# Optimization experiments

Hardware: AMD Instinct MI355X
Metric: run time of the kernel (lower is better)

Reference implementation:

```python
import jax, jax.numpy as jnp
import numpy as np

N, E, IN, HID, OUT, H, NCLS = 20000, 320000, 128, 32, 8, 8, 10

def _ln(x, g, b, eps=1e-5):
    mu = x.mean(-1, keepdims=True)
    var = ((x - mu) ** 2).mean(-1, keepdims=True)
    return g * (x - mu) / jnp.sqrt(var + eps) + b

def _gelu(x):
    return jax.nn.gelu(x, approximate=False)

def _tconv(x, src, dst, Wq, bq, Wk, bk, Wv, bv, Ws, bs, heads):
    # PyG TransformerConv, concat=True, root_weight=True, lin_beta is None
    n = x.shape[0]
    C = Wq.shape[1] // heads
    q = (x @ Wq + bq).reshape(n, heads, C)
    k = (x @ Wk + bk).reshape(n, heads, C)
    v = (x @ Wv + bv).reshape(n, heads, C)
    logits = (q[dst] * k[src]).sum(-1) / jnp.sqrt(jnp.asarray(C, x.dtype))  # [E,H]
    m = jax.lax.stop_gradient(jax.ops.segment_max(logits, dst, num_segments=n))
    e = jnp.exp(logits - m[dst])
    denom = jax.ops.segment_sum(e, dst, num_segments=n)
    alpha = e / (denom[dst] + 1e-16)  # per-target-node edge softmax
    agg = jax.ops.segment_sum(alpha[:, :, None] * v[src], dst, num_segments=n)
    out = agg.reshape(n, heads * C) + x @ Ws + bs
    return out, alpha

def _forward(src, dst, x,
             c1_Wq, c1_bq, c1_Wk, c1_bk, c1_Wv, c1_bv, c1_Ws, c1_bs,
             c2_Wq, c2_bq, c2_Wk, c2_bk, c2_Wv, c2_bv, c2_Ws, c2_bs,
             c3_Wq, c3_bq, c3_Wk, c3_bk, c3_Wv, c3_bv, c3_Ws, c3_bs,
             c4_Wq, c4_bq, c4_Wk, c4_bk, c4_Wv, c4_bv, c4_Ws, c4_bs,
             n1_g, n1_b, n2_g, n2_b, n3_g, n3_b, n4_g, n4_b,
             fc_W, fc_b):
    h1 = _ln(_gelu(_tconv(x, src, dst, c1_Wq, c1_bq, c1_Wk, c1_bk, c1_Wv, c1_bv, c1_Ws, c1_bs, H)[0]), n1_g, n1_b)
    h2_raw, attn = _tconv(h1, src, dst, c2_Wq, c2_bq, c2_Wk, c2_bk, c2_Wv, c2_bv, c2_Ws, c2_bs, H)
    h2 = _ln(_gelu(h2_raw), n2_g, n2_b)
    h3 = _ln(_gelu(_tconv(h2, src, dst, c3_Wq, c3_bq, c3_Wk, c3_bk, c3_Wv, c3_bv, c3_Ws, c3_bs, H)[0]), n3_g, n3_b)
    h4 = _ln(_gelu(_tconv(h3, src, dst, c4_Wq, c4_bq, c4_Wk, c4_bk, c4_Wv, c4_bv, c4_Ws, c4_bs, 1)[0]), n4_g, n4_b)
    x_out = h2 @ fc_W + fc_b
    return x_out, h4, attn

def setup_inputs() -> dict:
    key = jax.random.key(0)
    ks = iter(jax.random.split(key, 64))
    def p(shape, s=0.05):
        return jax.random.normal(next(ks), shape, dtype=jnp.float32) * s
    inp = {}
    inp['x'] = jax.random.normal(next(ks), (N, IN), dtype=jnp.float32)
    inp['edge_index'] = jax.random.randint(next(ks), (2, E), 0, N, dtype=jnp.int32)
    dims = [('c1', IN, H * HID), ('c2', H * HID, H * OUT), ('c3', H * OUT, H * HID), ('c4', H * HID, IN)]
    for name, di, do in dims:
        for w in ['Wq', 'Wk', 'Wv', 'Ws']:
            inp[name + '_' + w] = p((di, do))
        for bnm in ['bq', 'bk', 'bv', 'bs']:
            inp[name + '_' + bnm] = jnp.zeros((do,), jnp.float32)
    for nm, d in [('n1', H * HID), ('n2', H * OUT), ('n3', H * HID), ('n4', IN)]:
        inp[nm + '_g'] = jnp.ones((d,), jnp.float32)
        inp[nm + '_b'] = jnp.zeros((d,), jnp.float32)
    inp['fc_W'] = p((H * OUT, NCLS))
    inp['fc_b'] = jnp.zeros((NCLS,), jnp.float32)
    return inp

def reference(x, edge_index,
              c1_Wq, c1_bq, c1_Wk, c1_bk, c1_Wv, c1_bv, c1_Ws, c1_bs,
              c2_Wq, c2_bq, c2_Wk, c2_bk, c2_Wv, c2_bv, c2_Ws, c2_bs,
              c3_Wq, c3_bq, c3_Wk, c3_bk, c3_Wv, c3_bv, c3_Ws, c3_bs,
              c4_Wq, c4_bq, c4_Wk, c4_bk, c4_Wv, c4_bv, c4_Ws, c4_bs,
              n1_g, n1_b, n2_g, n2_b, n3_g, n3_b, n4_g, n4_b,
              fc_W, fc_b):
    src, dst = edge_index[0], edge_index[1]
    return _forward(src, dst, x,
                    c1_Wq, c1_bq, c1_Wk, c1_bk, c1_Wv, c1_bv, c1_Ws, c1_bs,
                    c2_Wq, c2_bq, c2_Wk, c2_bk, c2_Wv, c2_bv, c2_Ws, c2_bs,
                    c3_Wq, c3_bq, c3_Wk, c3_bk, c3_Wv, c3_bv, c3_Ws, c3_bs,
                    c4_Wq, c4_bq, c4_Wk, c4_bk, c4_Wv, c4_bv, c4_Ws, c4_bs,
                    n1_g, n1_b, n2_g, n2_b, n3_g, n3_b, n4_g, n4_b,
                    fc_W, fc_b)
```

## Files before the change

### kernel.cpp

```cpp
#include <hip/hip_runtime.h>
#include <hip/hip_bf16.h>
#include <math.h>

#define NN 20000
#define MP 20032
#define NE 320000

typedef __hip_bfloat16 bf16;
typedef __attribute__((ext_vector_type(8))) short short8v;
typedef __attribute__((ext_vector_type(4))) short short4v;
typedef __attribute__((ext_vector_type(4))) float f32x4;

__device__ __forceinline__ float b2f(bf16 v){ return __bfloat162float(v); }
__device__ __forceinline__ bf16 f2b(float v){ return __float2bfloat16(v); }
__device__ __forceinline__ float bfbits(short s){
  return __uint_as_float(((unsigned)(unsigned short)s) << 16);
}
__device__ __forceinline__ int clampi(int v, int lo, int hi){ return v < lo ? lo : (v > hi ? hi : v); }
__device__ __forceinline__ void stv(bf16* p, float v){ *p = f2b(v); }
__device__ __forceinline__ void stv(float* p, float v){ *p = v; }
__device__ __forceinline__ float ldv(const bf16* p){ return b2f(*p); }
__device__ __forceinline__ float ldv(const float* p){ return *p; }

template<int CPL>
__device__ __forceinline__ void ldrow(const bf16* p, float* o){
  if constexpr (CPL == 8){
    short8v v = *reinterpret_cast<const short8v*>(p);
#pragma unroll
    for (int j = 0; j < 8; j++) o[j] = bfbits(v[j]);
  } else {
    short4v v = *reinterpret_cast<const short4v*>(p);
#pragma unroll
    for (int j = 0; j < 4; j++) o[j] = bfbits(v[j]);
  }
}

__device__ __forceinline__ short8v ldA8(const bf16* p){
  return *reinterpret_cast<const short8v*>(p);
}
__device__ __forceinline__ short8v ldA8(const float* p){
  float4 a0 = *reinterpret_cast<const float4*>(p);
  float4 a1 = *reinterpret_cast<const float4*>(p + 4);
  short8v r;
  bf16 b;
  b = f2b(a0.x); r[0] = *(const short*)&b;
  b = f2b(a0.y); r[1] = *(const short*)&b;
  b = f2b(a0.z); r[2] = *(const short*)&b;
  b = f2b(a0.w); r[3] = *(const short*)&b;
  b = f2b(a1.x); r[4] = *(const short*)&b;
  b = f2b(a1.y); r[5] = *(const short*)&b;
  b = f2b(a1.z); r[6] = *(const short*)&b;
  b = f2b(a1.w); r[7] = *(const short*)&b;
  return r;
}

__global__ void fill_k(float* __restrict__ out, int n, float val){
  int i = blockIdx.x*blockDim.x + threadIdx.x;
  if (i < n) out[i] = val;
}

__global__ void pack_w(const float* __restrict__ W, bf16* __restrict__ Wp, int K, int D){
  int i = blockIdx.x*256 + threadIdx.x;
  if (i >= K*D) return;
  int j = i & 7, l = (i >> 3) & 63;
  int TG = D >> 4;
  int tg = (i >> 9) % TG, s = (i >> 9) / TG;
  int k = s*32 + (l >> 4)*8 + j, n = tg*16 + (l & 15);
  Wp[i] = f2b(W[(size_t)k*D + n]);
}

template<typename AT, typename TS>
__global__ void gemm_qkvs(const AT* __restrict__ X,
    const short8v* __restrict__ WQ, const short8v* __restrict__ WK,
    const short8v* __restrict__ WV, const short8v* __restrict__ WS,
    const float* __restrict__ bQ, const float* __restrict__ bK,
    const float* __restrict__ bV, const float* __restrict__ bS,
    bf16* __restrict__ Qo, bf16* __restrict__ Ko, bf16* __restrict__ Vo,
    TS* __restrict__ So,
    int K, int TG, int tg0, int ldQKV, int ldS, int ocolS, int MstoreS){
  int w = threadIdx.x >> 6, lane = threadIdx.x & 63;
  int n0 = blockIdx.x*64;
  size_t m0 = (size_t)blockIdx.y*64 + w*16;
  int lr = lane & 15, lk = lane >> 4;
  int ar = clampi((int)(m0 + lr), 0, NN-1);
  const AT* xp = X + (size_t)ar*K + lk*8;
  size_t wo = ((size_t)(tg0 + (n0 >> 4)))*64 + lane;
  f32x4 acc[4][4];
#pragma unroll
  for (int j = 0; j < 4; j++)
#pragma unroll
    for (int t = 0; t < 4; t++) acc[j][t] = f32x4{0,0,0,0};
  int steps = K >> 5;
  for (int s = 0; s < steps; s++){
    short8v a = ldA8(xp + s*32);
    size_t ro = wo + (size_t)s*TG*64;
#pragma unroll
    for (int t = 0; t < 4; t++){
      size_t idx = ro + t*64;
      acc[0][t] = __builtin_amdgcn_mfma_f32_16x16x32_bf16(a, WQ[idx], acc[0][t], 0, 0, 0);
      acc[1][t] = __builtin_amdgcn_mfma_f32_16x16x32_bf16(a, WK[idx], acc[1][t], 0, 0, 0);
      acc[2][t] = __builtin_amdgcn_mfma_f32_16x16x32_bf16(a, WV[idx], acc[2][t], 0, 0, 0);
      acc[3][t] = __builtin_amdgcn_mfma_f32_16x16x32_bf16(a, WS[idx], acc[3][t], 0, 0, 0);
    }
  }
#pragma unroll
  for (int t = 0; t < 4; t++){
    int col = n0 + t*16 + lr;
    float b0 = bQ[col], b1 = bK[col], b2 = bV[col], b3 = bS[col];
#pragma unroll
    for (int r = 0; r < 4; r++){
      size_t row = m0 + lk*4 + r;
      Qo[row*ldQKV + col] = f2b(acc[0][t][r] + b0);
      Ko[row*ldQKV + col] = f2b(acc[1][t][r] + b1);
      Vo[row*ldQKV + col] = f2b(acc[2][t][r] + b2);
      if ((int)row < MstoreS) stv(&So[row*(size_t)ldS + ocolS + col], acc[3][t][r] + b3);
    }
  }
}

__global__ void count_k(const int* __restrict__ ei, int* __restrict__ cnt, int E){
  int e = blockIdx.x*blockDim.x + threadIdx.x;
  if (e < E){
    int d = clampi(ei[E + e], 0, NN-1);
    atomicAdd(&cnt[d], 1);
  }
}

__global__ void exscan_k(const int* __restrict__ cnt, int* __restrict__ off, int n){
  __shared__ int wtot[16];
  __shared__ int carrysh;
  int tid = threadIdx.x, lane = tid & 63, w = tid >> 6;
  if (tid == 0) carrysh = 0;
  __syncthreads();
  for (int base = 0; base < n; base += 1024){
    int i = base + tid;
    int v = (i < n) ? cnt[i] : 0;
    int s = v;
#pragma unroll
    for (int d = 1; d < 64; d <<= 1){
      int t = __shfl_up(s, d);
      if (lane >= d) s += t;
    }
    if (lane == 63) wtot[w] = s;
    __syncthreads();
    int woff = 0;
    for (int j = 0; j < w; j++) woff += wtot[j];
    int c = carrysh;
    if (i < n) off[i] = c + woff + s - v;
    __syncthreads();
    if (tid == 1023) carrysh = c + woff + s;
    __syncthreads();
  }
  if (threadIdx.x == 0) off[n] = carrysh;
}

__global__ void scatter_k(const int* __restrict__ ei, int* __restrict__ cur,
                          int* __restrict__ perm, int* __restrict__ srcs, int E){
  int e = blockIdx.x*blockDim.x + threadIdx.x;
  if (e >= E) return;
  int s = clampi(ei[e], 0, NN-1);
  int d = clampi(ei[E + e], 0, NN-1);
  int p = atomicAdd(&cur[d], 1);
  if (p >= 0 && p < E){ perm[p] = e; srcs[p] = s; }
}

template<int D, int H, typename TO>
__global__ void fused_attn(const bf16* __restrict__ Q, const bf16* __restrict__ Kf,
                           const bf16* __restrict__ V, const int* __restrict__ srcs,
                           const int* __restrict__ offs,
                           TO* __restrict__ Xout, int ldO, int col0,
                           bf16* __restrict__ LOG, float* __restrict__ MxO,
                           float* __restrict__ DnO, float scale){
  constexpr int CPL = D/16;
  constexpr int LPH = 16/H;
  int node = blockIdx.x*4 + (threadIdx.x >> 6);
  if (node >= NN) return;
  int lane = threadIdx.x & 63;
  int hl = lane & 15;
  int slot = lane >> 4;
  float q[CPL];
  {
    float tmp[CPL];
    ldrow<CPL>(Q + (size_t)node*D + hl*CPL, tmp);
#pragma unroll
    for (int j = 0; j < CPL; j++) q[j] = tmp[j] * scale;
  }
  float m = -INFINITY, den = 0.f;
  float acc[CPL];
#pragma unroll
  for (int j = 0; j < CPL; j++) acc[j] = 0.f;
  int s0 = offs[node], e0 = offs[node+1];
  int i = s0 + slot;
  bool vcur = i < e0;
  int sc = vcur ? srcs[i] : 0;
  float kc[CPL], vc[CPL];
  ldrow<CPL>(Kf + (size_t)sc*D + hl*CPL, kc);
  ldrow<CPL>(V  + (size_t)sc*D + hl*CPL, vc);
  int iters = (e0 - s0 + 3) >> 2;
  for (int it = 0; it < iters; ++it){
    int inext = i + 4;
    bool vnxt = inext < e0;
    int sn = vnxt ? srcs[inext] : 0;
    float kn[CPL], vn[CPL];
    ldrow<CPL>(Kf + (size_t)sn*D + hl*CPL, kn);
    ldrow<CPL>(V  + (size_t)sn*D + hl*CPL, vn);
    float t = 0.f;
#pragma unroll
    for (int j = 0; j < CPL; j++) t += q[j]*kc[j];
#pragma unroll
    for (int o = 1; o < LPH; o <<= 1) t += __shfl_xor(t, o);
    if (!vcur) t = -INFINITY;
    if (LOG && vcur && ((hl & (LPH-1)) == 0)) LOG[(size_t)i*H + hl/LPH] = f2b(t);
    float tm = fmaxf(t, __shfl_xor(t, 16));
    tm = fmaxf(tm, __shfl_xor(tm, 32));
    float nm = fmaxf(m, tm);
    float fe = __expf(m - nm);
    float pe = __expf(t - nm);
    den = den*fe + pe;
#pragma unroll
    for (int j = 0; j < CPL; j++) acc[j] = acc[j]*fe + pe*vc[j];
    m = nm;
    vcur = vnxt; i = inext;
#pragma unroll
    for (int j = 0; j < CPL; j++){ kc[j] = kn[j]; vc[j] = vn[j]; }
  }
  den += __shfl_xor(den, 16);
  den += __shfl_xor(den, 32);
#pragma unroll
  for (int j = 0; j < CPL; j++){
    acc[j] += __shfl_xor(acc[j], 16);
    acc[j] += __shfl_xor(acc[j], 32);
  }
  float inv = 1.f/(den + 1e-16f);
  if (slot == 0){
    TO* o = Xout + (size_t)node*ldO + col0 + hl*CPL;
#pragma unroll
    for (int j = 0; j < CPL; j++) stv(&o[j], ldv(&o[j]) + acc[j]*inv);
    if (MxO && ((hl & (LPH-1)) == 0)){
      MxO[node*H + hl/LPH] = m;
      DnO[node*H + hl/LPH] = den;
    }
  }
}

__global__ void alpha8_k(const bf16* __restrict__ LOG, const float* __restrict__ Mx,
                         const float* __restrict__ Dn, const int* __restrict__ ei,
                         const int* __restrict__ perm, float* __restrict__ attn){
  size_t t = (size_t)blockIdx.x*blockDim.x + threadIdx.x;
  if (t >= (size_t)NE*8) return;
  int pos = (int)(t >> 3), h = (int)(t & 7);
  int e = perm[pos];
  int node = ei[NE + e];
  float a = __expf(b2f(LOG[t]) - Mx[node*8 + h]) / (Dn[node*8 + h] + 1e-16f);
  attn[(size_t)e*8 + h] = a;
}

template<int CPL, typename T>
__global__ void gelu_ln(T* __restrict__ X, const float* __restrict__ G,
                        const float* __restrict__ Bt){
  int node = blockIdx.x*4 + (threadIdx.x >> 6);
  if (node >= NN) return;
  constexpr int D = CPL*64;
  int lane = threadIdx.x & 63;
  T* xr = X + (size_t)node*D + lane*CPL;
  float v[CPL]; float s = 0.f;
#pragma unroll
  for (int j = 0; j < CPL; j++){
    float t = ldv(&xr[j]);
    float ge = 0.5f*t*(1.f + erff(t*0.70710678118654752f));
    v[j] = ge; s += ge;
  }
#pragma unroll
  for (int off = 1; off < 64; off <<= 1) s += __shfl_xor(s, off);
  float mu = s * (1.f/D);
  float q = 0.f;
#pragma unroll
  for (int j = 0; j < CPL; j++){ float d = v[j]-mu; q += d*d; }
#pragma unroll
  for (int off = 1; off < 64; off <<= 1) q += __shfl_xor(q, off);
  float inv = 1.f / sqrtf(q*(1.f/D) + 1e-5f);
#pragma unroll
  for (int j = 0; j < CPL; j++){
    int c = lane*CPL + j;
    stv(&xr[j], G[c]*(v[j]-mu)*inv + Bt[c]);
  }
}

__global__ void fc_k(const bf16* __restrict__ X, const float* __restrict__ W,
                     const float* __restrict__ B, float* __restrict__ Out,
                     int K, int D){
  int m = blockIdx.x*4 + (threadIdx.x >> 6);
  int lane = threadIdx.x & 63;
  if (m >= NN || lane >= D) return;
  float acc = B[lane];
  for (int k = 0; k < K; k++) acc += b2f(X[(size_t)m*K + k]) * W[(size_t)k*D + lane];
  Out[(size_t)m*D + lane] = acc;
}

extern "C" void kernel_launch(void* const* d_in, const int* in_sizes, int n_in,
                              void* d_out, int out_size, void* d_ws, size_t ws_size,
                              hipStream_t stream){
  int code = 0;
  if (n_in != 44) code = 100;
  else {
    const int wsz[4] = {32768,16384,16384,32768};
    const int bsz[4] = {256,64,256,128};
    bool ok = in_sizes[0] == NN*128 && in_sizes[1] == 2*NE
           && in_sizes[42] == 640 && in_sizes[43] == 10;
    for (int l = 0; l < 4 && ok; l++){
      for (int j = 0; j < 4; j++)
        ok = ok && in_sizes[2+l*8+j] == wsz[l] && in_sizes[2+l*8+4+j] == bsz[l];
      ok = ok && in_sizes[34+2*l] == bsz[l] && in_sizes[35+2*l] == bsz[l];
    }
    if (!ok) code = 140;
  }
  if (code){
    fill_k<<<((size_t)out_size+255)/256, 256, 0, stream>>>((float*)d_out, out_size, (float)code);
    return;
  }

  const float* x = (const float*)d_in[0];
  const int*   ei = (const int*)d_in[1];
  const float *W[4][4], *Bw[4][4], *lng[4], *lnb[4];
  for (int l = 0; l < 4; l++){
    for (int j = 0; j < 4; j++){
      W[l][j]  = (const float*)d_in[2 + l*8 + j];
      Bw[l][j] = (const float*)d_in[2 + l*8 + 4 + j];
    }
    lng[l] = (const float*)d_in[34 + 2*l];
    lnb[l] = (const float*)d_in[35 + 2*l];
  }
  const float* fcW = (const float*)d_in[42];
  const float* fcB = (const float*)d_in[43];

  char* ws = (char*)d_ws;
  size_t o = 0;
  auto alloc = [&](size_t bytes)->void*{ void* p = ws + o; o += (bytes + 255)/256*256; return p; };
  bf16* Hb   = (bf16*)alloc((size_t)MP*256*2);
  bf16* H2b  = (bf16*)alloc((size_t)MP*64*2);
  int* OFFS  = (int*)alloc((size_t)(NN+1)*4);
  int* PERM  = (int*)alloc((size_t)NE*4);
  int* SRCS  = (int*)alloc((size_t)NE*4);
  char* AR   = (char*)alloc((size_t)3*MP*128*2);
  bf16* WPK  = (bf16*)alloc((size_t)393216*2);
  size_t need = o;
  bf16* Qc = (bf16*)AR;
  bf16* Kc = (bf16*)(AR + (size_t)MP*128*2);
  bf16* Vc = (bf16*)(AR + (size_t)2*MP*128*2);
  int*  CURS = (int*)AR;
  bf16* q2  = (bf16*)AR;
  bf16* k2  = (bf16*)(AR + (size_t)MP*64*2);
  bf16* v2  = (bf16*)(AR + (size_t)2*MP*64*2);
  bf16* LOG = (bf16*)(AR + (size_t)3*MP*64*2);
  float* Mx = (float*)(AR + (size_t)3*MP*64*2 + (size_t)NE*8*2);
  float* Dn = (float*)((char*)Mx + (size_t)NN*8*4);

  float* out_x  = (float*)d_out;
  float* out_h4 = out_x + (size_t)NN*10;
  float* out_at = out_h4 + (size_t)NN*128;

  if (ws_size < need){
    fill_k<<<((size_t)out_size+255)/256, 256, 0, stream>>>((float*)d_out, out_size, 160.0f);
    return;
  }

  const int KD[4] = {128,256,64,256};
  const int DD[4] = {256,64,256,128};
  bf16* Wp[4][4];
  {
    size_t off = 0;
    for (int l = 0; l < 4; l++)
      for (int j = 0; j < 4; j++){
        Wp[l][j] = WPK + off;
        int kd = KD[l]*DD[l];
        pack_w<<<(kd+255)/256, 256, 0, stream>>>(W[l][j], Wp[l][j], KD[l], DD[l]);
        off += kd;
      }
  }

  hipMemsetAsync(CURS, 0, (size_t)NN*4, stream);
  count_k<<<NE/256, 256, 0, stream>>>(ei, CURS, NE);
  exscan_k<<<1, 1024, 0, stream>>>(CURS, OFFS, NN);
  hipMemcpyAsync(CURS, OFFS, (size_t)NN*4, hipMemcpyDeviceToDevice, stream);
  scatter_k<<<NE/256, 256, 0, stream>>>(ei, CURS, PERM, SRCS, NE);

  const float s32  = 0.1767766952966369f;
  const float s8   = 0.3535533905932738f;
  const float s128 = 0.0883883476483184f;
  const dim3 gm64(1, MP/64), gm128(2, MP/64);

  for (int col = 0; col <= 128; col += 128){
    int tg0 = col >> 4;
    gemm_qkvs<float,bf16><<<gm128,256,0,stream>>>(x,
        (const short8v*)Wp[0][0], (const short8v*)Wp[0][1],
        (const short8v*)Wp[0][2], (const short8v*)Wp[0][3],
        Bw[0][0]+col, Bw[0][1]+col, Bw[0][2]+col, Bw[0][3]+col,
        Qc, Kc, Vc, Hb, 128, 16, tg0, 128, 256, col, MP);
    fused_attn<128,4,bf16><<<NN/4,256,0,stream>>>(Qc,Kc,Vc, SRCS,OFFS, Hb,256,col,
                                                  nullptr,nullptr,nullptr, s32);
  }
  gelu_ln<4><<<NN/4,256,0,stream>>>(Hb, lng[0], lnb[0]);

  gemm_qkvs<bf16,bf16><<<gm64,256,0,stream>>>(Hb,
      (const short8v*)Wp[1][0], (const short8v*)Wp[1][1],
      (const short8v*)Wp[1][2], (const short8v*)Wp[1][3],
      Bw[1][0], Bw[1][1], Bw[1][2], Bw[1][3],
      q2, k2, v2, H2b, 256, 4, 0, 64, 64, 0, MP);
  fused_attn<64,8,bf16><<<NN/4,256,0,stream>>>(q2,k2,v2, SRCS,OFFS, H2b,64,0,
                                               LOG,Mx,Dn, s8);
  alpha8_k<<<NE*8/256,256,0,stream>>>(LOG, Mx, Dn, ei, PERM, out_at);
  gelu_ln<1><<<NN/4,256,0,stream>>>(H2b, lng[1], lnb[1]);

  fc_k<<<NN/4,256,0,stream>>>(H2b, fcW, fcB, out_x, 64, 10);

  for (int col = 0; col <= 128; col += 128){
    int tg0 = col >> 4;
    gemm_qkvs<bf16,bf16><<<gm128,256,0,stream>>>(H2b,
        (const short8v*)Wp[2][0], (const short8v*)Wp[2][1],
        (const short8v*)Wp[2][2], (const short8v*)Wp[2][3],
        Bw[2][0]+col, Bw[2][1]+col, Bw[2][2]+col, Bw[2][3]+col,
        Qc, Kc, Vc, Hb, 64, 16, tg0, 128, 256, col, MP);
    fused_attn<128,4,bf16><<<NN/4,256,0,stream>>>(Qc,Kc,Vc, SRCS,OFFS, Hb,256,col,
                                                  nullptr,nullptr,nullptr, s32);
  }
  gelu_ln<4><<<NN/4,256,0,stream>>>(Hb, lng[2], lnb[2]);

  gemm_qkvs<bf16,float><<<gm128,256,0,stream>>>(Hb,
      (const short8v*)Wp[3][0], (const short8v*)Wp[3][1],
      (const short8v*)Wp[3][2], (const short8v*)Wp[3][3],
      Bw[3][0], Bw[3][1], Bw[3][2], Bw[3][3],
      Qc, Kc, Vc, out_h4, 256, 8, 0, 128, 128, 0, NN);
  fused_attn<128,1,float><<<NN/4,256,0,stream>>>(Qc,Kc,Vc, SRCS,OFFS, out_h4,128,0,
                                                 nullptr,nullptr,nullptr, s128);
  gelu_ln<2><<<NN/4,256,0,stream>>>(out_h4, lng[3], lnb[3]);
}
```

Measured before the change: 398.2 us.

## Process full 256-wide layers in single passes and batch weight packing

Layers 1 and 3 previously ran as two 128-column halves, each with its own GEMM and attention pass. They now use one GEMM over all 256 columns and one fused attention with D=256 and CPL=16, so each edge's source indices, offsets and loop overhead are traversed once instead of twice. The 16 per-weight pack launches become a single pack_all launch, and the exscan writes the cursor array directly, which drops a device copy. Dedicated Q/K/V buffers replace the aliased scratch area, at the cost of more workspace and a higher register load per lane in attention.

New measurement: 364.4 us. -8.5%, faster.

```diff
diff --git a/kernel.cpp b/kernel.cpp
--- a/kernel.cpp
+++ b/kernel.cpp
@@ -24,7 +24,12 @@
 
 template<int CPL>
 __device__ __forceinline__ void ldrow(const bf16* p, float* o){
-  if constexpr (CPL == 8){
+  if constexpr (CPL == 16){
+    short8v v0 = *reinterpret_cast<const short8v*>(p);
+    short8v v1 = *reinterpret_cast<const short8v*>(p + 8);
+#pragma unroll
+    for (int j = 0; j < 8; j++){ o[j] = bfbits(v0[j]); o[8+j] = bfbits(v1[j]); }
+  } else if constexpr (CPL == 8){
     short8v v = *reinterpret_cast<const short8v*>(p);
 #pragma unroll
     for (int j = 0; j < 8; j++) o[j] = bfbits(v[j]);
@@ -59,14 +64,22 @@
   if (i < n) out[i] = val;
 }
 
-__global__ void pack_w(const float* __restrict__ W, bf16* __restrict__ Wp, int K, int D){
+struct PackArgs {
+  const float* w[16];
+  unsigned long long off[16];
+  int K[16];
+  int D[16];
+};
+__global__ void pack_all(PackArgs pa, bf16* __restrict__ out){
+  int wi = blockIdx.y;
+  int K = pa.K[wi], D = pa.D[wi];
   int i = blockIdx.x*256 + threadIdx.x;
   if (i >= K*D) return;
   int j = i & 7, l = (i >> 3) & 63;
   int TG = D >> 4;
   int tg = (i >> 9) % TG, s = (i >> 9) / TG;
   int k = s*32 + (l >> 4)*8 + j, n = tg*16 + (l & 15);
-  Wp[i] = f2b(W[(size_t)k*D + n]);
+  out[pa.off[wi] + i] = f2b(pa.w[wi][(size_t)k*D + n]);
 }
 
 template<typename AT, typename TS>
@@ -77,14 +90,14 @@
     const float* __restrict__ bV, const float* __restrict__ bS,
     bf16* __restrict__ Qo, bf16* __restrict__ Ko, bf16* __restrict__ Vo,
     TS* __restrict__ So,
-    int K, int TG, int tg0, int ldQKV, int ldS, int ocolS, int MstoreS){
+    int K, int TG, int ldQKV, int ldS, int MstoreS){
   int w = threadIdx.x >> 6, lane = threadIdx.x & 63;
   int n0 = blockIdx.x*64;
   size_t m0 = (size_t)blockIdx.y*64 + w*16;
   int lr = lane & 15, lk = lane >> 4;
   int ar = clampi((int)(m0 + lr), 0, NN-1);
   const AT* xp = X + (size_t)ar*K + lk*8;
-  size_t wo = ((size_t)(tg0 + (n0 >> 4)))*64 + lane;
+  size_t wo = ((size_t)(n0 >> 4))*64 + lane;
   f32x4 acc[4][4];
 #pragma unroll
   for (int j = 0; j < 4; j++)
@@ -113,7 +126,7 @@
       Qo[row*ldQKV + col] = f2b(acc[0][t][r] + b0);
       Ko[row*ldQKV + col] = f2b(acc[1][t][r] + b1);
       Vo[row*ldQKV + col] = f2b(acc[2][t][r] + b2);
-      if ((int)row < MstoreS) stv(&So[row*(size_t)ldS + ocolS + col], acc[3][t][r] + b3);
+      if ((int)row < MstoreS) stv(&So[row*(size_t)ldS + col], acc[3][t][r] + b3);
     }
   }
 }
@@ -126,7 +139,8 @@
   }
 }
 
-__global__ void exscan_k(const int* __restrict__ cnt, int* __restrict__ off, int n){
+__global__ void exscan_k(const int* __restrict__ cnt, int* __restrict__ off,
+                         int* __restrict__ cur, int n){
   __shared__ int wtot[16];
   __shared__ int carrysh;
   int tid = threadIdx.x, lane = tid & 63, w = tid >> 6;
@@ -146,7 +160,7 @@
     int woff = 0;
     for (int j = 0; j < w; j++) woff += wtot[j];
     int c = carrysh;
-    if (i < n) off[i] = c + woff + s - v;
+    if (i < n){ int val = c + woff + s - v; off[i] = val; cur[i] = val; }
     __syncthreads();
     if (tid == 1023) carrysh = c + woff + s;
     __syncthreads();
@@ -168,7 +182,7 @@
 __global__ void fused_attn(const bf16* __restrict__ Q, const bf16* __restrict__ Kf,
                            const bf16* __restrict__ V, const int* __restrict__ srcs,
                            const int* __restrict__ offs,
-                           TO* __restrict__ Xout, int ldO, int col0,
+                           TO* __restrict__ Xout, int ldO,
                            bf16* __restrict__ LOG, float* __restrict__ MxO,
                            float* __restrict__ DnO, float scale){
   constexpr int CPL = D/16;
@@ -233,7 +247,7 @@
   }
   float inv = 1.f/(den + 1e-16f);
   if (slot == 0){
-    TO* o = Xout + (size_t)node*ldO + col0 + hl*CPL;
+    TO* o = Xout + (size_t)node*ldO + hl*CPL;
 #pragma unroll
     for (int j = 0; j < CPL; j++) stv(&o[j], ldv(&o[j]) + acc[j]*inv);
     if (MxO && ((hl & (LPH-1)) == 0)){
@@ -338,22 +352,19 @@
   auto alloc = [&](size_t bytes)->void*{ void* p = ws + o; o += (bytes + 255)/256*256; return p; };
   bf16* Hb   = (bf16*)alloc((size_t)MP*256*2);
   bf16* H2b  = (bf16*)alloc((size_t)MP*64*2);
+  bf16* Qb   = (bf16*)alloc((size_t)MP*256*2);
+  bf16* Kb   = (bf16*)alloc((size_t)MP*256*2);
+  bf16* Vb   = (bf16*)alloc((size_t)MP*256*2);
+  bf16* LOG  = (bf16*)alloc((size_t)NE*8*2);
+  float* Mx  = (float*)alloc((size_t)NN*8*4);
+  float* Dn  = (float*)alloc((size_t)NN*8*4);
   int* OFFS  = (int*)alloc((size_t)(NN+1)*4);
+  int* CNT   = (int*)alloc((size_t)(NN+1)*4);
+  int* CURS  = (int*)alloc((size_t)(NN+1)*4);
   int* PERM  = (int*)alloc((size_t)NE*4);
   int* SRCS  = (int*)alloc((size_t)NE*4);
-  char* AR   = (char*)alloc((size_t)3*MP*128*2);
   bf16* WPK  = (bf16*)alloc((size_t)393216*2);
   size_t need = o;
-  bf16* Qc = (bf16*)AR;
-  bf16* Kc = (bf16*)(AR + (size_t)MP*128*2);
-  bf16* Vc = (bf16*)(AR + (size_t)2*MP*128*2);
-  int*  CURS = (int*)AR;
-  bf16* q2  = (bf16*)AR;
-  bf16* k2  = (bf16*)(AR + (size_t)MP*64*2);
-  bf16* v2  = (bf16*)(AR + (size_t)2*MP*64*2);
-  bf16* LOG = (bf16*)(AR + (size_t)3*MP*64*2);
-  float* Mx = (float*)(AR + (size_t)3*MP*64*2 + (size_t)NE*8*2);
-  float* Dn = (float*)((char*)Mx + (size_t)NN*8*4);
 
   float* out_x  = (float*)d_out;
   float* out_h4 = out_x + (size_t)NN*10;
@@ -366,71 +377,69 @@
 
   const int KD[4] = {128,256,64,256};
   const int DD[4] = {256,64,256,128};
+  PackArgs pa;
   bf16* Wp[4][4];
   {
     size_t off = 0;
     for (int l = 0; l < 4; l++)
       for (int j = 0; j < 4; j++){
+        int idx = l*4 + j;
+        pa.w[idx] = W[l][j];
+        pa.off[idx] = off;
+        pa.K[idx] = KD[l];
+        pa.D[idx] = DD[l];
         Wp[l][j] = WPK + off;
-        int kd = KD[l]*DD[l];
-        pack_w<<<(kd+255)/256, 256, 0, stream>>>(W[l][j], Wp[l][j], KD[l], DD[l]);
-        off += kd;
+        off += (size_t)KD[l]*DD[l];
       }
   }
-
-  hipMemsetAsync(CURS, 0, (size_t)NN*4, stream);
-  count_k<<<NE/256, 256, 0, stream>>>(ei, CURS, NE);
-  exscan_k<<<1, 1024, 0, stream>>>(CURS, OFFS, NN);
-  hipMemcpyAsync(CURS, OFFS, (size_t)NN*4, hipMemcpyDeviceToDevice, stream);
+  pack_all<<<dim3(128,16),256,0,stream>>>(pa, WPK);
+
+  hipMemsetAsync(CNT, 0, (size_t)NN*4, stream);
+  count_k<<<NE/256, 256, 0, stream>>>(ei, CNT, NE);
+  exscan_k<<<1, 1024, 0, stream>>>(CNT, OFFS, CURS, NN);
   scatter_k<<<NE/256, 256, 0, stream>>>(ei, CURS, PERM, SRCS, NE);
 
   const float s32  = 0.1767766952966369f;
   const float s8   = 0.3535533905932738f;
   const float s128 = 0.0883883476483184f;
-  const dim3 gm64(1, MP/64), gm128(2, MP/64);
-
-  for (int col = 0; col <= 128; col += 128){
-    int tg0 = col >> 4;
-    gemm_qkvs<float,bf16><<<gm128,256,0,stream>>>(x,
-        (const short8v*)Wp[0][0], (const short8v*)Wp[0][1],
-        (const short8v*)Wp[0][2], (const short8v*)Wp[0][3],
-        Bw[0][0]+col, Bw[0][1]+col, Bw[0][2]+col, Bw[0][3]+col,
-        Qc, Kc, Vc, Hb, 128, 16, tg0, 128, 256, col, MP);
-    fused_attn<128,4,bf16><<<NN/4,256,0,stream>>>(Qc,Kc,Vc, SRCS,OFFS, Hb,256,col,
-                                                  nullptr,nullptr,nullptr, s32);
-  }
+  const dim3 g64(1, MP/64), g128(2, MP/64), g256(4, MP/64);
+
+  gemm_qkvs<float,bf16><<<g256,256,0,stream>>>(x,
+      (const short8v*)Wp[0][0], (const short8v*)Wp[0][1],
+      (const short8v*)Wp[0][2], (const short8v*)Wp[0][3],
+      Bw[0][0], Bw[0][1], Bw[0][2], Bw[0][3],
+      Qb, Kb, Vb, Hb, 128, 16, 256, 256, MP);
+  fused_attn<256,8,bf16><<<NN/4,256,0,stream>>>(Qb,Kb,Vb, SRCS,OFFS, Hb,256,
+                                                nullptr,nullptr,nullptr, s32);
   gelu_ln<4><<<NN/4,256,0,stream>>>(Hb, lng[0], lnb[0]);
 
-  gemm_qkvs<bf16,bf16><<<gm64,256,0,stream>>>(Hb,
+  gemm_qkvs<bf16,bf16><<<g64,256,0,stream>>>(Hb,
       (const short8v*)Wp[1][0], (const short8v*)Wp[1][1],
       (const short8v*)Wp[1][2], (const short8v*)Wp[1][3],
       Bw[1][0], Bw[1][1], Bw[1][2], Bw[1][3],
-      q2, k2, v2, H2b, 256, 4, 0, 64, 64, 0, MP);
-  fused_attn<64,8,bf16><<<NN/4,256,0,stream>>>(q2,k2,v2, SRCS,OFFS, H2b,64,0,
+      Qb, Kb, Vb, H2b, 256, 4, 64, 64, MP);
+  fused_attn<64,8,bf16><<<NN/4,256,0,stream>>>(Qb,Kb,Vb, SRCS,OFFS, H2b,64,
                                                LOG,Mx,Dn, s8);
   alpha8_k<<<NE*8/256,256,0,stream>>>(LOG, Mx, Dn, ei, PERM, out_at);
   gelu_ln<1><<<NN/4,256,0,stream>>>(H2b, lng[1], lnb[1]);
 
   fc_k<<<NN/4,256,0,stream>>>(H2b, fcW, fcB, out_x, 64, 10);
 
-  for (int col = 0; col <= 128; col += 128){
-    int tg0 = col >> 4;
-    gemm_qkvs<bf16,bf16><<<gm128,256,0,stream>>>(H2b,
-        (const short8v*)Wp[2][0], (const short8v*)Wp[2][1],
-        (const short8v*)Wp[2][2], (const short8v*)Wp[2][3],
-        Bw[2][0]+col, Bw[2][1]+col, Bw[2][2]+col, Bw[2][3]+col,
-        Qc, Kc, Vc, Hb, 64, 16, tg0, 128, 256, col, MP);
-    fused_attn<128,4,bf16><<<NN/4,256,0,stream>>>(Qc,Kc,Vc, SRCS,OFFS, Hb,256,col,
-                                                  nullptr,nullptr,nullptr, s32);
-  }
+  gemm_qkvs<bf16,bf16><<<g256,256,0,stream>>>(H2b,
+      (const short8v*)Wp[2][0], (const short8v*)Wp[2][1],
+      (const short8v*)Wp[2][2], (const short8v*)Wp[2][3],
+      Bw[2][0], Bw[2][1], Bw[2][2], Bw[2][3],
+      Qb, Kb, Vb, Hb, 64, 16, 256, 256, MP);
+  fused_attn<256,8,bf16><<<NN/4,256,0,stream>>>(Qb,Kb,Vb, SRCS,OFFS, Hb,256,
+                                                nullptr,nullptr,nullptr, s32);
   gelu_ln<4><<<NN/4,256,0,stream>>>(Hb, lng[2], lnb[2]);
 
-  gemm_qkvs<bf16,float><<<gm128,256,0,stream>>>(Hb,
+  gemm_qkvs<bf16,float><<<g128,256,0,stream>>>(Hb,
       (const short8v*)Wp[3][0], (const short8v*)Wp[3][1],
       (const short8v*)Wp[3][2], (const short8v*)Wp[3][3],
       Bw[3][0], Bw[3][1], Bw[3][2], Bw[3][3],
-      Qc, Kc, Vc, out_h4, 256, 8, 0, 128, 128, 0, NN);
-  fused_attn<128,1,float><<<NN/4,256,0,stream>>>(Qc,Kc,Vc, SRCS,OFFS, out_h4,128,0,
+      Qb, Kb, Vb, out_h4, 256, 8, 128, 128, NN);
+  fused_attn<128,1,float><<<NN/4,256,0,stream>>>(Qb,Kb,Vb, SRCS,OFFS, out_h4,128,
                                                  nullptr,nullptr,nullptr, s128);
   gelu_ln<2><<<NN/4,256,0,stream>>>(out_h4, lng[3], lnb[3]);
 }
```
